# Kernel optimization log

Measured on AMD Instinct MI355X. Metric: run time of the kernel, lower is better.

The kernel has to match this reference:

```python
import jax, jax.numpy as jnp
import numpy as np

B, HW, FEAT = 64, 196, 2048
EMB, HID, ATT, VOCAB, T = 512, 1024, 512, 10000, 20
STEPS = T - 1  # pack_padded_sequence uses lengths - 1


def setup_inputs() -> dict:
    key = jax.random.key(0)
    ks = jax.random.split(key, 16)
    rn = lambda k, s, sc=0.02: jax.random.normal(k, s, jnp.float32) * sc
    return {
        "features": jax.random.normal(ks[0], (B, HW, FEAT), jnp.float32),
        "captions": jax.random.randint(ks[1], (B, T), 0, VOCAB),
        "lengths": jnp.full((B,), T, jnp.int32),  # uniform lengths -> constant batch per step
        "E": rn(ks[2], (VOCAB, EMB)),
        "W_feat": rn(ks[3], (EMB, FEAT)), "b_feat": jnp.zeros((EMB,), jnp.float32),
        "W1": rn(ks[4], (ATT, EMB)), "b1": jnp.zeros((ATT,), jnp.float32),
        "W2": rn(ks[5], (ATT, HID)), "b2": jnp.zeros((ATT,), jnp.float32),
        "V": rn(ks[6], (1, ATT)), "bV": jnp.zeros((1,), jnp.float32),
        "W_hi": rn(ks[7], (HID, EMB)), "b_hi": jnp.zeros((HID,), jnp.float32),
        "W_ci": rn(ks[8], (HID, EMB)), "b_ci": jnp.zeros((HID,), jnp.float32),
        "W_ih": rn(ks[9], (4 * HID, 2 * EMB)), "b_ih": jnp.zeros((4 * HID,), jnp.float32),
        "W_hh": rn(ks[10], (4 * HID, HID)), "b_hh": jnp.zeros((4 * HID,), jnp.float32),
        "W_out": rn(ks[11], (VOCAB, HID)), "b_out": jnp.zeros((VOCAB,), jnp.float32),
    }


def reference(features, captions, lengths, E, W_feat, b_feat, W1, b1, W2, b2,
              V, bV, W_hi, b_hi, W_ci, b_ci, W_ih, b_ih, W_hh, b_hh, W_out, b_out):
    # features -> embed space: [B, HW, EMB]
    f = jnp.einsum('bhc,ec->bhe', features, W_feat) + b_feat
    fmean = f.mean(axis=1)                      # [B, EMB]
    hx0 = fmean @ W_hi.T + b_hi                 # [B, HID]
    cx0 = fmean @ W_ci.T + b_ci                 # [B, HID]
    fa = jnp.einsum('bhe,ae->bha', f, W1) + b1  # W1(features), [B, HW, ATT]

    emb = E[captions]                           # [B, T, EMB]
    xs = jnp.swapaxes(emb[:, :STEPS], 0, 1)     # [STEPS, B, EMB] teacher-forced inputs

    def step(carry, x):
        hx, cx = carry
        # Bahdanau attention
        ha = hx @ W2.T + b2                             # [B, ATT]
        score = jnp.tanh(fa + ha[:, None, :])           # [B, HW, ATT]
        logits = jnp.einsum('bha,oa->bho', score, V) + bV   # [B, HW, 1]
        w = jax.nn.softmax(logits, axis=1)              # softmax over HW
        ctx = jnp.sum(w * f, axis=1)                    # [B, EMB]
        # LSTMCell (PyTorch gate order: i, f, g, o)
        inp = jnp.concatenate([x, ctx], axis=1)         # [B, 2*EMB]
        gates = inp @ W_ih.T + b_ih + hx @ W_hh.T + b_hh
        i_g, f_g, g_g, o_g = jnp.split(gates, 4, axis=1)
        cx_n = jax.nn.sigmoid(f_g) * cx + jax.nn.sigmoid(i_g) * jnp.tanh(g_g)
        hx_n = jax.nn.sigmoid(o_g) * jnp.tanh(cx_n)
        out = hx_n @ W_out.T + b_out                    # dropout = identity (eval)
        return (hx_n, cx_n), out

    _, outs = jax.lax.scan(step, (hx0, cx0), xs)        # [STEPS, B, VOCAB]
    # torch.cat(outputs) over constant per-step batch == flatten time-major
    return outs.reshape(STEPS * B, VOCAB)
```

## Files before the change

### kernel.cpp

```cpp
#include <hip/hip_runtime.h>
#include <hip/hip_bf16.h>
#include <math.h>

#define BB 64
#define HW 196
#define FEAT 2048
#define EMB 512
#define HID 1024
#define ATT 512
#define VOCAB 10000
#define TT 20
#define STEPS 19

using bfrag = __attribute__((ext_vector_type(8))) short;
using f32x4 = __attribute__((ext_vector_type(4))) float;

__device__ __forceinline__ float sigmoid_fast(float x) { return 1.0f / (1.0f + __expf(-x)); }
__device__ __forceinline__ float tanh_fast(float x) {
    float e = __expf(2.0f * x);
    return 1.0f - 2.0f / (e + 1.0f);
}
__device__ __forceinline__ ushort f2bf_rne(float f) {
    unsigned u = __float_as_uint(f);
    unsigned r = (u + 0x7FFFu + ((u >> 16) & 1u)) >> 16;
    return (ushort)r;
}
__device__ __forceinline__ float bf2f(ushort h) {
    return __uint_as_float(((unsigned)h) << 16);
}
__device__ __forceinline__ int sw_idx(int row, int g) { return row * 4 + (g ^ ((row >> 1) & 3)); }

__global__ __launch_bounds__(256) void k_split(const float* __restrict__ x,
                                               ushort* __restrict__ hi,
                                               ushort* __restrict__ lo, int n)
{
    int i4 = (blockIdx.x * 256 + threadIdx.x) * 4;
    if (i4 >= n) return;
    float4 v = *(const float4*)(x + i4);
    float av[4] = {v.x, v.y, v.z, v.w};
    #pragma unroll
    for (int j = 0; j < 4; ++j) {
        ushort h = f2bf_rne(av[j]);
        hi[i4 + j] = h;
        lo[i4 + j] = f2bf_rne(av[j] - bf2f(h));
    }
}

__global__ __launch_bounds__(256) void k_cvt(const float* __restrict__ x,
                                             ushort* __restrict__ y, int n)
{
    int i4 = (blockIdx.x * 256 + threadIdx.x) * 4;
    if (i4 >= n) return;
    float4 v = *(const float4*)(x + i4);
    *(ushort4*)(y + i4) = make_ushort4(f2bf_rne(v.x), f2bf_rne(v.y),
                                       f2bf_rne(v.z), f2bf_rne(v.w));
}

template<bool NFAST, bool GLDS>
__global__ __launch_bounds__(256) void mfma_g(
    const float* __restrict__ A,
    const ushort* __restrict__ Bhi, const ushort* __restrict__ Blo,
    const float* __restrict__ bias, float* __restrict__ C,
    int N, int K, int Bld, int ldc, int NXB, int NMB)
{
    __shared__ __align__(16) ushort sAh[256 * 8];
    __shared__ __align__(16) ushort sAl[256 * 8];
    __shared__ __align__(16) ushort sBh[512 * 8];
    __shared__ __align__(16) ushort sBl[512 * 8];

    const int tid = threadIdx.x;

    const int nwg = NXB * NMB;
    const int q = nwg >> 3, r = nwg & 7;
    const int xcd = blockIdx.x & 7, sidx = blockIdx.x >> 3;
    const int wg = (xcd < r) ? (xcd * (q + 1) + sidx)
                             : (r * (q + 1) + (xcd - r) * q + sidx);
    int im, inb;
    if (NFAST) { inb = wg % NXB; im = wg / NXB; }
    else       { im = wg % NMB; inb = wg / NMB; }
    const int m0 = im * 64;
    const int n0 = inb * 128;

    const int lane = tid & 63;
    const int w = tid >> 6;
    const int mh = (w & 1) * 32;
    const int nh = (w >> 1) * 64;
    const int g = lane >> 4, l15 = lane & 15;

    const ushort* bsrc[4];
    ushort* bdst[4];
    if (GLDS) {
        #pragma unroll
        for (int i = 0; i < 4; ++i) {
            int cbase = i * 256 + w * 64;
            int plane = cbase >> 9;
            int ccb = cbase & 511;
            int cc = ccb + lane;
            int row = cc >> 2;
            int g_ = (cc & 3) ^ ((row >> 1) & 3);
            int brow = min(n0 + row, N - 1);
            bsrc[i] = (plane ? Blo : Bhi) + (size_t)brow * Bld + g_ * 8;
            bdst[i] = (plane ? sBl : sBh) + ccb * 8;
        }
    }

    f32x4 acc[2][4] = {};

    for (int k0 = 0; k0 < K; k0 += 32) {
        __syncthreads();
        {
            int r_ = tid >> 2, g_ = tid & 3;
            const float* ap = A + (size_t)(m0 + r_) * K + k0 + g_ * 8;
            float av[8];
            *(float4*)(av)     = *(const float4*)(ap);
            *(float4*)(av + 4) = *(const float4*)(ap + 4);
            bfrag vh, vl;
            #pragma unroll
            for (int j = 0; j < 8; ++j) {
                ushort h = f2bf_rne(av[j]);
                vh[j] = (short)h;
                vl[j] = (short)f2bf_rne(av[j] - bf2f(h));
            }
            int c = sw_idx(r_, g_) * 8;
            *(bfrag*)&sAh[c] = vh;
            *(bfrag*)&sAl[c] = vl;
        }
        if (GLDS) {
            #pragma unroll
            for (int i = 0; i < 4; ++i)
                __builtin_amdgcn_global_load_lds(
                    (const __attribute__((address_space(1))) void*)(bsrc[i] + k0),
                    (__attribute__((address_space(3))) void*)bdst[i], 16, 0, 0);
        } else {
            #pragma unroll
            for (int i = 0; i < 4; ++i) {
                int c = tid + i * 256;
                int pl = c >> 9, idx2 = c & 511;
                int r_ = idx2 >> 2, g_ = idx2 & 3;
                int brow = min(n0 + r_, N - 1);
                const ushort* src = (pl ? Blo : Bhi) + (size_t)brow * Bld + k0 + g_ * 8;
                int cc = sw_idx(r_, g_) * 8;
                if (pl) *(bfrag*)&sBl[cc] = *(const bfrag*)src;
                else    *(bfrag*)&sBh[cc] = *(const bfrag*)src;
            }
        }
        __syncthreads();

        bfrag ah[2], al[2], bh[4], bl[4];
        #pragma unroll
        for (int s = 0; s < 2; ++s) {
            int c = sw_idx(mh + s * 16 + l15, g) * 8;
            ah[s] = *(const bfrag*)&sAh[c];
            al[s] = *(const bfrag*)&sAl[c];
        }
        #pragma unroll
        for (int u = 0; u < 4; ++u) {
            int c = sw_idx(nh + u * 16 + l15, g) * 8;
            bh[u] = *(const bfrag*)&sBh[c];
            bl[u] = *(const bfrag*)&sBl[c];
        }
        #pragma unroll
        for (int s = 0; s < 2; ++s)
            #pragma unroll
            for (int u = 0; u < 4; ++u) {
                acc[s][u] = __builtin_amdgcn_mfma_f32_16x16x32_bf16(ah[s], bh[u], acc[s][u], 0, 0, 0);
                acc[s][u] = __builtin_amdgcn_mfma_f32_16x16x32_bf16(ah[s], bl[u], acc[s][u], 0, 0, 0);
                acc[s][u] = __builtin_amdgcn_mfma_f32_16x16x32_bf16(al[s], bh[u], acc[s][u], 0, 0, 0);
            }
    }

    #pragma unroll
    for (int s = 0; s < 2; ++s)
        #pragma unroll
        for (int u = 0; u < 4; ++u) {
            int col = n0 + nh + u * 16 + l15;
            if (col < N) {
                float bv = bias ? bias[col] : 0.f;
                #pragma unroll
                for (int rr = 0; rr < 4; ++rr) {
                    int row = m0 + mh + s * 16 + g * 4 + rr;
                    C[(size_t)row * ldc + col] = acc[s][u][rr] + bv;
                }
            }
        }
}

__global__ __launch_bounds__(256) void k_fmean2(const float* __restrict__ f,
                                                float* __restrict__ fmean)
{
    __shared__ float part[128];
    int blk = blockIdx.x;
    int b = blk >> 2, eq = blk & 3;
    int el = threadIdx.x & 127, half = threadIdx.x >> 7;
    int e = eq * 128 + el;
    const float* fb = f + (size_t)b * HW * EMB + e;
    float s = 0.f;
    int h0 = half * 98;
    for (int h = h0; h < h0 + 98; ++h) s += fb[(size_t)h * EMB];
    if (half) part[el] = s;
    __syncthreads();
    if (!half) fmean[b * EMB + e] = (s + part[el]) * (1.0f / HW);
}

__global__ __launch_bounds__(256) void k_init2(
    const float* __restrict__ fmean,
    const float* __restrict__ W_hi, const float* __restrict__ b_hi,
    const float* __restrict__ W_ci, const float* __restrict__ b_ci,
    float* __restrict__ hx, float* __restrict__ cx,
    ushort* __restrict__ hxp_h, ushort* __restrict__ hxp_l)
{
    int o = blockIdx.x * 256 + threadIdx.x;
    int b = o >> 11, uu = o & 2047;
    bool isC = uu >= 1024;
    int u = uu & 1023;
    const float4* wr = (const float4*)((isC ? W_ci : W_hi) + (size_t)u * EMB);
    const float4* fm = (const float4*)(fmean + (size_t)b * EMB);
    float s = isC ? b_ci[u] : b_hi[u];
    #pragma unroll 8
    for (int k = 0; k < EMB / 4; ++k) {
        float4 wv = wr[k], xv = fm[k];
        s += wv.x*xv.x + wv.y*xv.y + wv.z*xv.z + wv.w*xv.w;
    }
    int idx = b * HID + u;
    if (isC) cx[idx] = s;
    else {
        hx[idx] = s;
        ushort hh = f2bf_rne(s);
        hxp_h[idx] = hh;
        hxp_l[idx] = f2bf_rne(s - bf2f(hh));
    }
}

__global__ __launch_bounds__(128) void k_embed(const int* __restrict__ cap,
                                               const float* __restrict__ E,
                                               float* __restrict__ xs_f)
{
    int blk = blockIdx.x;
    int t = blk / BB, b = blk % BB;
    int c = cap[b * TT + t];
    const float4* src = (const float4*)(E + (size_t)c * EMB);
    float4* dst = (float4*)(xs_f + ((size_t)t * BB + b) * EMB);
    dst[threadIdx.x] = src[threadIdx.x];
}

__global__ __launch_bounds__(256) void k_ha(
    const float* __restrict__ hx, const float* __restrict__ W2,
    const float* __restrict__ b2, float* __restrict__ ha)
{
    __shared__ __align__(16) float hx_s[8][1028];
    __shared__ float part[256];
    const int tid = threadIdx.x;
    const int a0 = (blockIdx.x >> 3) * 16;
    const int b0 = (blockIdx.x & 7) * 8;

    for (int i = tid; i < 8 * 256; i += 256) {
        int r = i >> 8, c4 = i & 255;
        *(float4*)&hx_s[r][c4 * 4] = *(const float4*)(hx + (size_t)(b0 + r) * HID + c4 * 4);
    }
    __syncthreads();

    const int a_i = tid >> 4;
    const int b_i = (tid >> 1) & 7;
    const int half = tid & 1;
    const float4* wr = (const float4*)(W2 + (size_t)(a0 + a_i) * HID + half * 512);
    const float* xr = &hx_s[b_i][half * 512];
    float s = 0.f;
    #pragma unroll 8
    for (int i = 0; i < 128; ++i) {
        float4 w = wr[i];
        float4 x = *(const float4*)(xr + i * 4);
        s += w.x*x.x + w.y*x.y + w.z*x.z + w.w*x.w;
    }
    part[tid] = s;
    __syncthreads();
    if (!half)
        ha[(size_t)(b0 + b_i) * ATT + a0 + a_i] = part[tid] + part[tid + 1] + b2[a0 + a_i];
}

__global__ __launch_bounds__(1024) void k_att(
    const ushort* __restrict__ f16, const ushort* __restrict__ fa16,
    const float* __restrict__ ha, const float* __restrict__ V,
    ushort* __restrict__ ctx_hi, ushort* __restrict__ ctx_lo)
{
    __shared__ __align__(16) float smem[2048];
    const int b = blockIdx.x;
    const int tid = threadIdx.x;
    const int lane = tid & 63;
    const int wid = tid >> 6;

    float* ha_s = smem;
    float* V_s  = smem + 512;
    float* w_s  = smem + 1024;
    float* red  = smem + 1280;
    float* pc   = smem + 1536;

    if (tid < ATT) { ha_s[tid] = ha[b * ATT + tid]; V_s[tid] = V[tid]; }
    __syncthreads();

    for (int h = wid; h < HW; h += 16) {
        bfrag fv = *(const bfrag*)(fa16 + ((size_t)b * HW + h) * ATT + lane * 8);
        const float* hp = &ha_s[lane * 8];
        const float* vp = &V_s[lane * 8];
        float s = 0.f;
        #pragma unroll
        for (int j = 0; j < 8; ++j)
            s += tanh_fast(bf2f((ushort)fv[j]) + hp[j]) * vp[j];
        #pragma unroll
        for (int off = 32; off > 0; off >>= 1) s += __shfl_down(s, off);
        if (lane == 0) w_s[h] = s;
    }
    __syncthreads();

    float v = (tid < HW) ? w_s[tid] : -INFINITY;
    if (tid < 256) red[tid] = v;
    __syncthreads();
    for (int s2 = 128; s2 > 0; s2 >>= 1) {
        if (tid < s2) red[tid] = fmaxf(red[tid], red[tid + s2]);
        __syncthreads();
    }
    float mx = red[0];
    __syncthreads();
    float e = (tid < HW) ? __expf(v - mx) : 0.f;
    if (tid < 256) red[tid] = e;
    __syncthreads();
    for (int s2 = 128; s2 > 0; s2 >>= 1) {
        if (tid < s2) red[tid] += red[tid + s2];
        __syncthreads();
    }
    float inv = 1.0f / red[0];
    if (tid < HW) w_s[tid] = e * inv;
    __syncthreads();

    {
        int e0 = tid & 511, grp = tid >> 9;
        const ushort* fb = f16 + (size_t)b * HW * EMB + e0;
        float s = 0.f;
        int h0 = grp * 98;
        for (int h = h0; h < h0 + 98; ++h)
            s = fmaf(w_s[h], bf2f(fb[(size_t)h * EMB]), s);
        if (grp) pc[e0] = s;
        __syncthreads();
        if (!grp) {
            float c = s + pc[e0];
            ushort ch = f2bf_rne(c);
            ctx_hi[b * EMB + e0] = ch;
            ctx_lo[b * EMB + e0] = f2bf_rne(c - bf2f(ch));
        }
    }
}

__global__ __launch_bounds__(512) void k_gates_lstm(
    const float* __restrict__ gxs_t,
    const ushort* __restrict__ cth, const ushort* __restrict__ ctl,
    const ushort* __restrict__ hxh, const ushort* __restrict__ hxl,
    const ushort* __restrict__ wihh, const ushort* __restrict__ wihl,
    const ushort* __restrict__ whhh, const ushort* __restrict__ whhl,
    const float* __restrict__ b_ih, const float* __restrict__ b_hh,
    float* __restrict__ hx, float* __restrict__ cx,
    ushort* __restrict__ nxh, ushort* __restrict__ nxl,
    float* __restrict__ hx_all_t)
{
    __shared__ float sg[2][64][16];
    const int tid = threadIdx.x, bk = blockIdx.x;
    const int lane = tid & 63, wid = tid >> 6;
    const int mt = wid & 3, kh = wid >> 2;
    const int l15 = lane & 15, g = lane >> 4;
    const int arow = mt * 16 + l15;
    const int ncol = (l15 >> 2) * 1024 + bk * 4 + (l15 & 3);
    const int koff = g * 8;

    f32x4 acc0 = {}, acc1 = {};

    if (kh == 0) {
        {
            const ushort* ah = cth + (size_t)arow * 512 + koff;
            const ushort* al = ctl + (size_t)arow * 512 + koff;
            const ushort* bh = wihh + (size_t)ncol * 1024 + 512 + koff;
            const ushort* bl = wihl + (size_t)ncol * 1024 + 512 + koff;
            #pragma unroll 4
            for (int kk = 0; kk < 16; ++kk) {
                bfrag a_h = *(const bfrag*)(ah + kk * 32);
                bfrag a_l = *(const bfrag*)(al + kk * 32);
                bfrag b_h = *(const bfrag*)(bh + kk * 32);
                bfrag b_l = *(const bfrag*)(bl + kk * 32);
                acc0 = __builtin_amdgcn_mfma_f32_16x16x32_bf16(a_h, b_h, acc0, 0, 0, 0);
                acc1 = __builtin_amdgcn_mfma_f32_16x16x32_bf16(a_h, b_l, acc1, 0, 0, 0);
                acc1 = __builtin_amdgcn_mfma_f32_16x16x32_bf16(a_l, b_h, acc1, 0, 0, 0);
            }
        }
        {
            const ushort* ah = hxh + (size_t)arow * 1024 + koff;
            const ushort* al = hxl + (size_t)arow * 1024 + koff;
            const ushort* bh = whhh + (size_t)ncol * 1024 + koff;
            const ushort* bl = whhl + (size_t)ncol * 1024 + koff;
            #pragma unroll 4
            for (int kk = 0; kk < 8; ++kk) {
                bfrag a_h = *(const bfrag*)(ah + kk * 32);
                bfrag a_l = *(const bfrag*)(al + kk * 32);
                bfrag b_h = *(const bfrag*)(bh + kk * 32);
                bfrag b_l = *(const bfrag*)(bl + kk * 32);
                acc0 = __builtin_amdgcn_mfma_f32_16x16x32_bf16(a_h, b_h, acc0, 0, 0, 0);
                acc1 = __builtin_amdgcn_mfma_f32_16x16x32_bf16(a_h, b_l, acc1, 0, 0, 0);
                acc1 = __builtin_amdgcn_mfma_f32_16x16x32_bf16(a_l, b_h, acc1, 0, 0, 0);
            }
        }
    } else {
        const ushort* ah = hxh + (size_t)arow * 1024 + 256 + koff;
        const ushort* al = hxl + (size_t)arow * 1024 + 256 + koff;
        const ushort* bh = whhh + (size_t)ncol * 1024 + 256 + koff;
        const ushort* bl = whhl + (size_t)ncol * 1024 + 256 + koff;
        #pragma unroll 4
        for (int kk = 0; kk < 24; ++kk) {
            bfrag a_h = *(const bfrag*)(ah + kk * 32);
            bfrag a_l = *(const bfrag*)(al + kk * 32);
            bfrag b_h = *(const bfrag*)(bh + kk * 32);
            bfrag b_l = *(const bfrag*)(bl + kk * 32);
            acc0 = __builtin_amdgcn_mfma_f32_16x16x32_bf16(a_h, b_h, acc0, 0, 0, 0);
            acc1 = __builtin_amdgcn_mfma_f32_16x16x32_bf16(a_h, b_l, acc1, 0, 0, 0);
            acc1 = __builtin_amdgcn_mfma_f32_16x16x32_bf16(a_l, b_h, acc1, 0, 0, 0);
        }
    }

    #pragma unroll
    for (int rr = 0; rr < 4; ++rr)
        sg[kh][mt * 16 + g * 4 + rr][l15] = acc0[rr] + acc1[rr];
    __syncthreads();

    if (tid < 256) {
        int b = tid >> 2, uu = tid & 3;
        int u = bk * 4 + uu;
        const float* gx = gxs_t + (size_t)b * 4096;
        float gi = sg[0][b][uu]      + sg[1][b][uu]      + gx[u]        + b_ih[u]        + b_hh[u];
        float gf = sg[0][b][4 + uu]  + sg[1][b][4 + uu]  + gx[1024 + u] + b_ih[1024 + u] + b_hh[1024 + u];
        float gg = sg[0][b][8 + uu]  + sg[1][b][8 + uu]  + gx[2048 + u] + b_ih[2048 + u] + b_hh[2048 + u];
        float go = sg[0][b][12 + uu] + sg[1][b][12 + uu] + gx[3072 + u] + b_ih[3072 + u] + b_hh[3072 + u];
        int idx = b * 1024 + u;
        float c = sigmoid_fast(gf) * cx[idx] + sigmoid_fast(gi) * tanh_fast(gg);
        float h = sigmoid_fast(go) * tanh_fast(c);
        cx[idx] = c;
        hx[idx] = h;
        hx_all_t[idx] = h;
        ushort hh = f2bf_rne(h);
        nxh[idx] = hh;
        nxl[idx] = f2bf_rne(h - bf2f(hh));
    }
}

extern "C" void kernel_launch(void* const* d_in, const int* in_sizes, int n_in,
                              void* d_out, int out_size, void* d_ws, size_t ws_size,
                              hipStream_t stream) {
    const float* features = (const float*)d_in[0];
    const int*   captions = (const int*)d_in[1];
    const float* E      = (const float*)d_in[3];
    const float* W_feat = (const float*)d_in[4];
    const float* b_feat = (const float*)d_in[5];
    const float* W1     = (const float*)d_in[6];
    const float* b1     = (const float*)d_in[7];
    const float* W2     = (const float*)d_in[8];
    const float* b2     = (const float*)d_in[9];
    const float* V      = (const float*)d_in[10];
    const float* W_hi   = (const float*)d_in[12];
    const float* b_hi   = (const float*)d_in[13];
    const float* W_ci   = (const float*)d_in[14];
    const float* b_ci   = (const float*)d_in[15];
    const float* W_ih   = (const float*)d_in[16];
    const float* b_ih   = (const float*)d_in[17];
    const float* W_hh   = (const float*)d_in[18];
    const float* b_hh   = (const float*)d_in[19];
    const float* W_out  = (const float*)d_in[20];
    const float* b_out  = (const float*)d_in[21];
    float* out = (float*)d_out;

    float* ws = (float*)d_ws;
    float* f_buf   = ws;
    float* fa_buf  = f_buf + 6422528;
    float* fmean   = fa_buf + 6422528;
    float* hx      = fmean + 32768;
    float* cx      = hx + 65536;
    float* hx_all  = cx + 65536;
    float* ha      = hx_all + 1310720;
    float* xs_f    = ha + 32768;
    float* gxs     = xs_f + 622592;
    ushort* p = (ushort*)(gxs + 4980736);
    ushort* wfeat_hi = p;            p += 1048576;
    ushort* wfeat_lo = p;            p += 1048576;
    ushort* w1_hi    = p;            p += 262144;
    ushort* w1_lo    = p;            p += 262144;
    ushort* wih_hi   = p;            p += 4194304;
    ushort* wih_lo   = p;            p += 4194304;
    ushort* whh_hi   = p;            p += 4194304;
    ushort* whh_lo   = p;            p += 4194304;
    ushort* ctx_hi   = p;            p += 32768;
    ushort* ctx_lo   = p;            p += 32768;
    ushort* hxp      = p;            p += 262144;
    ushort* f16      = p;            p += 6422528;
    ushort* fa16     = p;            p += 6422528;
    ushort* wout_hi = (ushort*)f_buf;
    ushort* wout_lo = wout_hi + 10240000;

    k_split<<<1048576 / 4 / 256, 256, 0, stream>>>(W_feat, wfeat_hi, wfeat_lo, 1048576);
    k_split<<<262144 / 4 / 256, 256, 0, stream>>>(W1, w1_hi, w1_lo, 262144);
    k_split<<<4194304 / 4 / 256, 256, 0, stream>>>(W_ih, wih_hi, wih_lo, 4194304);
    k_split<<<4194304 / 4 / 256, 256, 0, stream>>>(W_hh, whh_hi, whh_lo, 4194304);
    k_embed<<<STEPS * BB, 128, 0, stream>>>(captions, E, xs_f);
    mfma_g<true, true><<<784, 256, 0, stream>>>(
        features, wfeat_hi, wfeat_lo, b_feat, f_buf, 512, 2048, 2048, 512, 4, 196);
    mfma_g<true, false><<<784, 256, 0, stream>>>(
        f_buf, w1_hi, w1_lo, b1, fa_buf, 512, 512, 512, 512, 4, 196);
    mfma_g<false, false><<<608, 256, 0, stream>>>(
        xs_f, wih_hi, wih_lo, nullptr, gxs, 4096, 512, 1024, 4096, 32, 19);
    k_cvt<<<6422528 / 4 / 256, 256, 0, stream>>>(f_buf, f16, 6422528);
    k_cvt<<<6422528 / 4 / 256, 256, 0, stream>>>(fa_buf, fa16, 6422528);
    k_fmean2<<<256, 256, 0, stream>>>(f_buf, fmean);
    k_init2<<<512, 256, 0, stream>>>(fmean, W_hi, b_hi, W_ci, b_ci,
                                     hx, cx, hxp, hxp + 65536);

    for (int t = 0; t < STEPS; ++t) {
        ushort* hx_rd = hxp + (size_t)(t & 1) * 131072;
        ushort* hx_wr = hxp + (size_t)((t + 1) & 1) * 131072;
        k_ha<<<256, 256, 0, stream>>>(hx, W2, b2, ha);
        k_att<<<BB, 1024, 0, stream>>>(f16, fa16, ha, V, ctx_hi, ctx_lo);
        k_gates_lstm<<<256, 512, 0, stream>>>(
            gxs + (size_t)t * BB * 4096,
            ctx_hi, ctx_lo, hx_rd, hx_rd + 65536,
            wih_hi, wih_lo, whh_hi, whh_lo, b_ih, b_hh,
            hx, cx, hx_wr, hx_wr + 65536,
            hx_all + (size_t)t * BB * HID);
    }

    k_split<<<10240000 / 4 / 256, 256, 0, stream>>>(W_out, wout_hi, wout_lo, 10240000);
    mfma_g<false, false><<<1501, 256, 0, stream>>>(
        hx_all, wout_hi, wout_lo, b_out, out, VOCAB, HID, 1024, VOCAB, 79, 19);
}
```

Before: 1.578 ms.

## Fuse recurrent step kernels into one persistent kernel with grid barriers

Replaces the per-step launches of the attention-projection, attention and LSTM-gate kernels (57 launches) with a single persistent 256-block kernel. Inside it, a hierarchical atomic grid barrier separates the phases. Attention is now split across 4 blocks per batch row: one phase writes logits to global memory, and a later phase does the softmax and context, replacing the old 64-block attention kernel. The aim is to remove launch overhead and make better use of the GPU in the attention phase. In exchange it adds four grid barriers per step and relies on all 256 blocks being co-resident, or the kernel deadlocks.

Result: slower. 2.054 ms (+30.2%).

```diff
diff --git a/kernel.cpp b/kernel.cpp
--- a/kernel.cpp
+++ b/kernel.cpp
@@ -243,206 +243,239 @@
     dst[threadIdx.x] = src[threadIdx.x];
 }
 
-__global__ __launch_bounds__(256) void k_ha(
-    const float* __restrict__ hx, const float* __restrict__ W2,
-    const float* __restrict__ b2, float* __restrict__ ha)
-{
-    __shared__ __align__(16) float hx_s[8][1028];
-    __shared__ float part[256];
-    const int tid = threadIdx.x;
-    const int a0 = (blockIdx.x >> 3) * 16;
-    const int b0 = (blockIdx.x & 7) * 8;
-
-    for (int i = tid; i < 8 * 256; i += 256) {
-        int r = i >> 8, c4 = i & 255;
-        *(float4*)&hx_s[r][c4 * 4] = *(const float4*)(hx + (size_t)(b0 + r) * HID + c4 * 4);
-    }
+__global__ void k_bar_init(int* bar) { bar[threadIdx.x] = 0; }
+
+__device__ __forceinline__ void gbar(int* bar) {
     __syncthreads();
-
-    const int a_i = tid >> 4;
-    const int b_i = (tid >> 1) & 7;
-    const int half = tid & 1;
-    const float4* wr = (const float4*)(W2 + (size_t)(a0 + a_i) * HID + half * 512);
-    const float* xr = &hx_s[b_i][half * 512];
-    float s = 0.f;
-    #pragma unroll 8
-    for (int i = 0; i < 128; ++i) {
-        float4 w = wr[i];
-        float4 x = *(const float4*)(xr + i * 4);
-        s += w.x*x.x + w.y*x.y + w.z*x.z + w.w*x.w;
-    }
-    part[tid] = s;
+    if (threadIdx.x == 0) {
+        __threadfence();
+        int* gen  = bar;
+        int* rcnt = bar + 32;
+        int* gcnt = bar + 64 + (blockIdx.x & 15) * 32;
+        int g = __hip_atomic_load(gen, __ATOMIC_RELAXED, __HIP_MEMORY_SCOPE_AGENT);
+        bool done = false;
+        if (__hip_atomic_fetch_add(gcnt, 1, __ATOMIC_RELAXED, __HIP_MEMORY_SCOPE_AGENT) == 15) {
+            __hip_atomic_store(gcnt, 0, __ATOMIC_RELAXED, __HIP_MEMORY_SCOPE_AGENT);
+            if (__hip_atomic_fetch_add(rcnt, 1, __ATOMIC_RELAXED, __HIP_MEMORY_SCOPE_AGENT) == 15) {
+                __hip_atomic_store(rcnt, 0, __ATOMIC_RELAXED, __HIP_MEMORY_SCOPE_AGENT);
+                __hip_atomic_fetch_add(gen, 1, __ATOMIC_RELEASE, __HIP_MEMORY_SCOPE_AGENT);
+                done = true;
+            }
+        }
+        if (!done)
+            while (__hip_atomic_load(gen, __ATOMIC_RELAXED, __HIP_MEMORY_SCOPE_AGENT) == g)
+                __builtin_amdgcn_s_sleep(1);
+        __builtin_amdgcn_fence(__ATOMIC_ACQUIRE, "agent");
+    }
     __syncthreads();
-    if (!half)
-        ha[(size_t)(b0 + b_i) * ATT + a0 + a_i] = part[tid] + part[tid + 1] + b2[a0 + a_i];
-}
-
-__global__ __launch_bounds__(1024) void k_att(
+}
+
+__global__ __launch_bounds__(512) void k_steps(
     const ushort* __restrict__ f16, const ushort* __restrict__ fa16,
-    const float* __restrict__ ha, const float* __restrict__ V,
-    ushort* __restrict__ ctx_hi, ushort* __restrict__ ctx_lo)
-{
-    __shared__ __align__(16) float smem[2048];
-    const int b = blockIdx.x;
-    const int tid = threadIdx.x;
-    const int lane = tid & 63;
-    const int wid = tid >> 6;
-
-    float* ha_s = smem;
-    float* V_s  = smem + 512;
-    float* w_s  = smem + 1024;
-    float* red  = smem + 1280;
-    float* pc   = smem + 1536;
-
-    if (tid < ATT) { ha_s[tid] = ha[b * ATT + tid]; V_s[tid] = V[tid]; }
-    __syncthreads();
-
-    for (int h = wid; h < HW; h += 16) {
-        bfrag fv = *(const bfrag*)(fa16 + ((size_t)b * HW + h) * ATT + lane * 8);
-        const float* hp = &ha_s[lane * 8];
-        const float* vp = &V_s[lane * 8];
-        float s = 0.f;
-        #pragma unroll
-        for (int j = 0; j < 8; ++j)
-            s += tanh_fast(bf2f((ushort)fv[j]) + hp[j]) * vp[j];
-        #pragma unroll
-        for (int off = 32; off > 0; off >>= 1) s += __shfl_down(s, off);
-        if (lane == 0) w_s[h] = s;
-    }
-    __syncthreads();
-
-    float v = (tid < HW) ? w_s[tid] : -INFINITY;
-    if (tid < 256) red[tid] = v;
-    __syncthreads();
-    for (int s2 = 128; s2 > 0; s2 >>= 1) {
-        if (tid < s2) red[tid] = fmaxf(red[tid], red[tid + s2]);
-        __syncthreads();
-    }
-    float mx = red[0];
-    __syncthreads();
-    float e = (tid < HW) ? __expf(v - mx) : 0.f;
-    if (tid < 256) red[tid] = e;
-    __syncthreads();
-    for (int s2 = 128; s2 > 0; s2 >>= 1) {
-        if (tid < s2) red[tid] += red[tid + s2];
-        __syncthreads();
-    }
-    float inv = 1.0f / red[0];
-    if (tid < HW) w_s[tid] = e * inv;
-    __syncthreads();
-
-    {
-        int e0 = tid & 511, grp = tid >> 9;
-        const ushort* fb = f16 + (size_t)b * HW * EMB + e0;
-        float s = 0.f;
-        int h0 = grp * 98;
-        for (int h = h0; h < h0 + 98; ++h)
-            s = fmaf(w_s[h], bf2f(fb[(size_t)h * EMB]), s);
-        if (grp) pc[e0] = s;
-        __syncthreads();
-        if (!grp) {
-            float c = s + pc[e0];
-            ushort ch = f2bf_rne(c);
-            ctx_hi[b * EMB + e0] = ch;
-            ctx_lo[b * EMB + e0] = f2bf_rne(c - bf2f(ch));
-        }
-    }
-}
-
-__global__ __launch_bounds__(512) void k_gates_lstm(
-    const float* __restrict__ gxs_t,
-    const ushort* __restrict__ cth, const ushort* __restrict__ ctl,
-    const ushort* __restrict__ hxh, const ushort* __restrict__ hxl,
+    const float* __restrict__ W2, const float* __restrict__ b2,
+    const float* __restrict__ V,
+    const float* __restrict__ gxs,
     const ushort* __restrict__ wihh, const ushort* __restrict__ wihl,
     const ushort* __restrict__ whhh, const ushort* __restrict__ whhl,
     const float* __restrict__ b_ih, const float* __restrict__ b_hh,
+    float* __restrict__ ha, float* __restrict__ logits,
+    ushort* __restrict__ cth, ushort* __restrict__ ctl,
+    ushort* __restrict__ hxp,
     float* __restrict__ hx, float* __restrict__ cx,
-    ushort* __restrict__ nxh, ushort* __restrict__ nxl,
-    float* __restrict__ hx_all_t)
-{
-    __shared__ float sg[2][64][16];
-    const int tid = threadIdx.x, bk = blockIdx.x;
-    const int lane = tid & 63, wid = tid >> 6;
-    const int mt = wid & 3, kh = wid >> 2;
-    const int l15 = lane & 15, g = lane >> 4;
-    const int arow = mt * 16 + l15;
-    const int ncol = (l15 >> 2) * 1024 + bk * 4 + (l15 & 3);
-    const int koff = g * 8;
-
-    f32x4 acc0 = {}, acc1 = {};
-
-    if (kh == 0) {
+    float* __restrict__ hx_all, int* __restrict__ bar)
+{
+    __shared__ __align__(16) float smem[8736];
+    const int tid = threadIdx.x;
+    const int blk = blockIdx.x;
+    const int lane = tid & 63;
+
+    for (int t = 0; t < STEPS; ++t) {
         {
-            const ushort* ah = cth + (size_t)arow * 512 + koff;
-            const ushort* al = ctl + (size_t)arow * 512 + koff;
-            const ushort* bh = wihh + (size_t)ncol * 1024 + 512 + koff;
-            const ushort* bl = wihl + (size_t)ncol * 1024 + 512 + koff;
-            #pragma unroll 4
-            for (int kk = 0; kk < 16; ++kk) {
-                bfrag a_h = *(const bfrag*)(ah + kk * 32);
-                bfrag a_l = *(const bfrag*)(al + kk * 32);
-                bfrag b_h = *(const bfrag*)(bh + kk * 32);
-                bfrag b_l = *(const bfrag*)(bl + kk * 32);
-                acc0 = __builtin_amdgcn_mfma_f32_16x16x32_bf16(a_h, b_h, acc0, 0, 0, 0);
-                acc1 = __builtin_amdgcn_mfma_f32_16x16x32_bf16(a_h, b_l, acc1, 0, 0, 0);
-                acc1 = __builtin_amdgcn_mfma_f32_16x16x32_bf16(a_l, b_h, acc1, 0, 0, 0);
-            }
-        }
+            const int a0 = (blk >> 3) * 16;
+            const int b0 = (blk & 7) * 8;
+            float* hx_s = smem;
+            float* part = smem + 8224;
+            for (int i = tid; i < 8 * 256; i += 512) {
+                int r = i >> 8, c4 = i & 255;
+                *(float4*)&hx_s[r * 1028 + c4 * 4] =
+                    *(const float4*)(hx + (size_t)(b0 + r) * HID + c4 * 4);
+            }
+            __syncthreads();
+            int a_i = tid >> 5, b_i = (tid >> 2) & 7, qq = tid & 3;
+            const float4* wr = (const float4*)(W2 + (size_t)(a0 + a_i) * HID + qq * 256);
+            const float* xr = &hx_s[b_i * 1028 + qq * 256];
+            float s = 0.f;
+            #pragma unroll 8
+            for (int i = 0; i < 64; ++i) {
+                float4 w = wr[i];
+                float4 x = *(const float4*)(xr + i * 4);
+                s += w.x*x.x + w.y*x.y + w.z*x.z + w.w*x.w;
+            }
+            part[tid] = s;
+            __syncthreads();
+            if (qq == 0)
+                ha[(size_t)(b0 + b_i) * ATT + a0 + a_i] =
+                    part[tid] + part[tid + 1] + part[tid + 2] + part[tid + 3] + b2[a0 + a_i];
+        }
+        gbar(bar);
+
         {
-            const ushort* ah = hxh + (size_t)arow * 1024 + koff;
-            const ushort* al = hxl + (size_t)arow * 1024 + koff;
-            const ushort* bh = whhh + (size_t)ncol * 1024 + koff;
-            const ushort* bl = whhl + (size_t)ncol * 1024 + koff;
-            #pragma unroll 4
-            for (int kk = 0; kk < 8; ++kk) {
-                bfrag a_h = *(const bfrag*)(ah + kk * 32);
-                bfrag a_l = *(const bfrag*)(al + kk * 32);
-                bfrag b_h = *(const bfrag*)(bh + kk * 32);
-                bfrag b_l = *(const bfrag*)(bl + kk * 32);
-                acc0 = __builtin_amdgcn_mfma_f32_16x16x32_bf16(a_h, b_h, acc0, 0, 0, 0);
-                acc1 = __builtin_amdgcn_mfma_f32_16x16x32_bf16(a_h, b_l, acc1, 0, 0, 0);
-                acc1 = __builtin_amdgcn_mfma_f32_16x16x32_bf16(a_l, b_h, acc1, 0, 0, 0);
-            }
-        }
-    } else {
-        const ushort* ah = hxh + (size_t)arow * 1024 + 256 + koff;
-        const ushort* al = hxl + (size_t)arow * 1024 + 256 + koff;
-        const ushort* bh = whhh + (size_t)ncol * 1024 + 256 + koff;
-        const ushort* bl = whhl + (size_t)ncol * 1024 + 256 + koff;
-        #pragma unroll 4
-        for (int kk = 0; kk < 24; ++kk) {
-            bfrag a_h = *(const bfrag*)(ah + kk * 32);
-            bfrag a_l = *(const bfrag*)(al + kk * 32);
-            bfrag b_h = *(const bfrag*)(bh + kk * 32);
-            bfrag b_l = *(const bfrag*)(bl + kk * 32);
-            acc0 = __builtin_amdgcn_mfma_f32_16x16x32_bf16(a_h, b_h, acc0, 0, 0, 0);
-            acc1 = __builtin_amdgcn_mfma_f32_16x16x32_bf16(a_h, b_l, acc1, 0, 0, 0);
-            acc1 = __builtin_amdgcn_mfma_f32_16x16x32_bf16(a_l, b_h, acc1, 0, 0, 0);
-        }
-    }
-
-    #pragma unroll
-    for (int rr = 0; rr < 4; ++rr)
-        sg[kh][mt * 16 + g * 4 + rr][l15] = acc0[rr] + acc1[rr];
-    __syncthreads();
-
-    if (tid < 256) {
-        int b = tid >> 2, uu = tid & 3;
-        int u = bk * 4 + uu;
-        const float* gx = gxs_t + (size_t)b * 4096;
-        float gi = sg[0][b][uu]      + sg[1][b][uu]      + gx[u]        + b_ih[u]        + b_hh[u];
-        float gf = sg[0][b][4 + uu]  + sg[1][b][4 + uu]  + gx[1024 + u] + b_ih[1024 + u] + b_hh[1024 + u];
-        float gg = sg[0][b][8 + uu]  + sg[1][b][8 + uu]  + gx[2048 + u] + b_ih[2048 + u] + b_hh[2048 + u];
-        float go = sg[0][b][12 + uu] + sg[1][b][12 + uu] + gx[3072 + u] + b_ih[3072 + u] + b_hh[3072 + u];
-        int idx = b * 1024 + u;
-        float c = sigmoid_fast(gf) * cx[idx] + sigmoid_fast(gi) * tanh_fast(gg);
-        float h = sigmoid_fast(go) * tanh_fast(c);
-        cx[idx] = c;
-        hx[idx] = h;
-        hx_all_t[idx] = h;
-        ushort hh = f2bf_rne(h);
-        nxh[idx] = hh;
-        nxl[idx] = f2bf_rne(h - bf2f(hh));
+            const int b = blk >> 2, qh = blk & 3;
+            float* ha_s = smem;
+            float* V_s  = smem + 512;
+            if (tid < ATT) { ha_s[tid] = ha[b * ATT + tid]; V_s[tid] = V[tid]; }
+            __syncthreads();
+            int wid = tid >> 6;
+            for (int h = qh * 49 + wid; h < qh * 49 + 49; h += 8) {
+                bfrag fv = *(const bfrag*)(fa16 + ((size_t)b * HW + h) * ATT + lane * 8);
+                const float* hp = &ha_s[lane * 8];
+                const float* vp = &V_s[lane * 8];
+                float s = 0.f;
+                #pragma unroll
+                for (int j = 0; j < 8; ++j)
+                    s += tanh_fast(bf2f((ushort)fv[j]) + hp[j]) * vp[j];
+                #pragma unroll
+                for (int off = 32; off > 0; off >>= 1) s += __shfl_down(s, off);
+                if (lane == 0) logits[b * HW + h] = s;
+            }
+        }
+        gbar(bar);
+
+        {
+            const int b = blk >> 2, eq = blk & 3;
+            float* w_s  = smem;
+            float* red  = smem + 256;
+            float* part = smem + 768;
+            float v = (tid < HW) ? logits[b * HW + tid] : -INFINITY;
+            red[tid] = v;
+            __syncthreads();
+            for (int s2 = 256; s2 > 0; s2 >>= 1) {
+                if (tid < s2) red[tid] = fmaxf(red[tid], red[tid + s2]);
+                __syncthreads();
+            }
+            float mx = red[0];
+            __syncthreads();
+            float e = (tid < HW) ? __expf(v - mx) : 0.f;
+            red[tid] = e;
+            __syncthreads();
+            for (int s2 = 256; s2 > 0; s2 >>= 1) {
+                if (tid < s2) red[tid] += red[tid + s2];
+                __syncthreads();
+            }
+            float inv = 1.0f / red[0];
+            if (tid < HW) w_s[tid] = e * inv;
+            __syncthreads();
+            int el = tid & 127, hg = tid >> 7;
+            int e0 = eq * 128 + el;
+            const ushort* fb = f16 + (size_t)b * HW * EMB + e0;
+            float s = 0.f;
+            int h0 = hg * 49;
+            for (int h = h0; h < h0 + 49; ++h)
+                s = fmaf(w_s[h], bf2f(fb[(size_t)h * EMB]), s);
+            part[tid] = s;
+            __syncthreads();
+            if (hg == 0) {
+                float c = s + part[tid + 128] + part[tid + 256] + part[tid + 384];
+                ushort ch = f2bf_rne(c);
+                cth[b * EMB + e0] = ch;
+                ctl[b * EMB + e0] = f2bf_rne(c - bf2f(ch));
+            }
+        }
+        gbar(bar);
+
+        {
+            const ushort* hxh = hxp + (size_t)(t & 1) * 131072;
+            const ushort* hxl = hxh + 65536;
+            ushort* nxh = hxp + (size_t)((t + 1) & 1) * 131072;
+            ushort* nxl = nxh + 65536;
+            const float* gxs_t = gxs + (size_t)t * BB * 4096;
+            float* hx_all_t = hx_all + (size_t)t * BB * HID;
+            float (*sg)[64][16] = (float(*)[64][16])smem;
+
+            const int wid = tid >> 6;
+            const int mt = wid & 3, kh = wid >> 2;
+            const int l15 = lane & 15, g = lane >> 4;
+            const int arow = mt * 16 + l15;
+            const int ncol = (l15 >> 2) * 1024 + blk * 4 + (l15 & 3);
+            const int koff = g * 8;
+
+            f32x4 acc0 = {}, acc1 = {};
+
+            if (kh == 0) {
+                {
+                    const ushort* ah = cth + (size_t)arow * 512 + koff;
+                    const ushort* al = ctl + (size_t)arow * 512 + koff;
+                    const ushort* bh = wihh + (size_t)ncol * 1024 + 512 + koff;
+                    const ushort* bl = wihl + (size_t)ncol * 1024 + 512 + koff;
+                    #pragma unroll 4
+                    for (int kk = 0; kk < 16; ++kk) {
+                        bfrag a_h = *(const bfrag*)(ah + kk * 32);
+                        bfrag a_l = *(const bfrag*)(al + kk * 32);
+                        bfrag b_h = *(const bfrag*)(bh + kk * 32);
+                        bfrag b_l = *(const bfrag*)(bl + kk * 32);
+                        acc0 = __builtin_amdgcn_mfma_f32_16x16x32_bf16(a_h, b_h, acc0, 0, 0, 0);
+                        acc1 = __builtin_amdgcn_mfma_f32_16x16x32_bf16(a_h, b_l, acc1, 0, 0, 0);
+                        acc1 = __builtin_amdgcn_mfma_f32_16x16x32_bf16(a_l, b_h, acc1, 0, 0, 0);
+                    }
+                }
+                {
+                    const ushort* ah = hxh + (size_t)arow * 1024 + koff;
+                    const ushort* al = hxl + (size_t)arow * 1024 + koff;
+                    const ushort* bh = whhh + (size_t)ncol * 1024 + koff;
+                    const ushort* bl = whhl + (size_t)ncol * 1024 + koff;
+                    #pragma unroll 4
+                    for (int kk = 0; kk < 8; ++kk) {
+                        bfrag a_h = *(const bfrag*)(ah + kk * 32);
+                        bfrag a_l = *(const bfrag*)(al + kk * 32);
+                        bfrag b_h = *(const bfrag*)(bh + kk * 32);
+                        bfrag b_l = *(const bfrag*)(bl + kk * 32);
+                        acc0 = __builtin_amdgcn_mfma_f32_16x16x32_bf16(a_h, b_h, acc0, 0, 0, 0);
+                        acc1 = __builtin_amdgcn_mfma_f32_16x16x32_bf16(a_h, b_l, acc1, 0, 0, 0);
+                        acc1 = __builtin_amdgcn_mfma_f32_16x16x32_bf16(a_l, b_h, acc1, 0, 0, 0);
+                    }
+                }
+            } else {
+                const ushort* ah = hxh + (size_t)arow * 1024 + 256 + koff;
+                const ushort* al = hxl + (size_t)arow * 1024 + 256 + koff;
+                const ushort* bh = whhh + (size_t)ncol * 1024 + 256 + koff;
+                const ushort* bl = whhl + (size_t)ncol * 1024 + 256 + koff;
+                #pragma unroll 4
+                for (int kk = 0; kk < 24; ++kk) {
+                    bfrag a_h = *(const bfrag*)(ah + kk * 32);
+                    bfrag a_l = *(const bfrag*)(al + kk * 32);
+                    bfrag b_h = *(const bfrag*)(bh + kk * 32);
+                    bfrag b_l = *(const bfrag*)(bl + kk * 32);
+                    acc0 = __builtin_amdgcn_mfma_f32_16x16x32_bf16(a_h, b_h, acc0, 0, 0, 0);
+                    acc1 = __builtin_amdgcn_mfma_f32_16x16x32_bf16(a_h, b_l, acc1, 0, 0, 0);
+                    acc1 = __builtin_amdgcn_mfma_f32_16x16x32_bf16(a_l, b_h, acc1, 0, 0, 0);
+                }
+            }
+
+            #pragma unroll
+            for (int rr = 0; rr < 4; ++rr)
+                sg[kh][mt * 16 + g * 4 + rr][l15] = acc0[rr] + acc1[rr];
+            __syncthreads();
+
+            if (tid < 256) {
+                int b = tid >> 2, uu = tid & 3;
+                int u = blk * 4 + uu;
+                const float* gx = gxs_t + (size_t)b * 4096;
+                float gi = sg[0][b][uu]      + sg[1][b][uu]      + gx[u]        + b_ih[u]        + b_hh[u];
+                float gf = sg[0][b][4 + uu]  + sg[1][b][4 + uu]  + gx[1024 + u] + b_ih[1024 + u] + b_hh[1024 + u];
+                float gg = sg[0][b][8 + uu]  + sg[1][b][8 + uu]  + gx[2048 + u] + b_ih[2048 + u] + b_hh[2048 + u];
+                float go = sg[0][b][12 + uu] + sg[1][b][12 + uu] + gx[3072 + u] + b_ih[3072 + u] + b_hh[3072 + u];
+                int idx = b * 1024 + u;
+                float c = sigmoid_fast(gf) * cx[idx] + sigmoid_fast(gi) * tanh_fast(gg);
+                float h = sigmoid_fast(go) * tanh_fast(c);
+                cx[idx] = c;
+                hx[idx] = h;
+                hx_all_t[idx] = h;
+                ushort hh = f2bf_rne(h);
+                nxh[idx] = hh;
+                nxl[idx] = f2bf_rne(h - bf2f(hh));
+            }
+        }
+        if (t != STEPS - 1) gbar(bar);
     }
 }
 
@@ -479,9 +512,11 @@
     float* cx      = hx + 65536;
     float* hx_all  = cx + 65536;
     float* ha      = hx_all + 1310720;
-    float* xs_f    = ha + 32768;
+    float* logits  = ha + 32768;
+    float* xs_f    = logits + 16384;
     float* gxs     = xs_f + 622592;
-    ushort* p = (ushort*)(gxs + 4980736);
+    int*   bar     = (int*)(gxs + 4980736);
+    ushort* p = (ushort*)(bar + 1024);
     ushort* wfeat_hi = p;            p += 1048576;
     ushort* wfeat_lo = p;            p += 1048576;
     ushort* w1_hi    = p;            p += 262144;
@@ -498,6 +533,7 @@
     ushort* wout_hi = (ushort*)f_buf;
     ushort* wout_lo = wout_hi + 10240000;
 
+    k_bar_init<<<1, 1024, 0, stream>>>(bar);
     k_split<<<1048576 / 4 / 256, 256, 0, stream>>>(W_feat, wfeat_hi, wfeat_lo, 1048576);
     k_split<<<262144 / 4 / 256, 256, 0, stream>>>(W1, w1_hi, w1_lo, 262144);
     k_split<<<4194304 / 4 / 256, 256, 0, stream>>>(W_ih, wih_hi, wih_lo, 4194304);
@@ -515,18 +551,10 @@
     k_init2<<<512, 256, 0, stream>>>(fmean, W_hi, b_hi, W_ci, b_ci,
                                      hx, cx, hxp, hxp + 65536);
 
-    for (int t = 0; t < STEPS; ++t) {
-        ushort* hx_rd = hxp + (size_t)(t & 1) * 131072;
-        ushort* hx_wr = hxp + (size_t)((t + 1) & 1) * 131072;
-        k_ha<<<256, 256, 0, stream>>>(hx, W2, b2, ha);
-        k_att<<<BB, 1024, 0, stream>>>(f16, fa16, ha, V, ctx_hi, ctx_lo);
-        k_gates_lstm<<<256, 512, 0, stream>>>(
-            gxs + (size_t)t * BB * 4096,
-            ctx_hi, ctx_lo, hx_rd, hx_rd + 65536,
-            wih_hi, wih_lo, whh_hi, whh_lo, b_ih, b_hh,
-            hx, cx, hx_wr, hx_wr + 65536,
-            hx_all + (size_t)t * BB * HID);
-    }
+    k_steps<<<256, 512, 0, stream>>>(
+        f16, fa16, W2, b2, V, gxs,
+        wih_hi, wih_lo, whh_hi, whh_lo, b_ih, b_hh,
+        ha, logits, ctx_hi, ctx_lo, hxp, hx, cx, hx_all, bar);
 
     k_split<<<10240000 / 4 / 256, 256, 0, stream>>>(W_out, wout_hi, wout_lo, 10240000);
     mfma_g<false, false><<<1501, 256, 0, stream>>>(
```
